# Optimization experiments

Hardware: AMD Instinct MI355X
Metric: run time of the kernel (lower is better)

Reference implementation:

```python
import jax, jax.numpy as jnp
import numpy as np

B, P, K = 8, 1024, 20          # clouds, points per cloud, knn neighbors
H, HD = 256, 512               # module hidden_dim, edge-MLP hidden (TransformerBlockRes default)
L, C = 3, 512                  # n_hidden_layers, n_components
N = B * P
LN_EPS = 1e-5


def _layer_norm(x, g, b):
    m = jnp.mean(x, axis=-1, keepdims=True)
    v = jnp.var(x, axis=-1, keepdims=True)
    return (x - m) * jax.lax.rsqrt(v + LN_EPS) * g + b


def _mlp(x, W1, b1, g1, be1, W2, b2, g2, be2):
    # Linear -> LayerNorm -> ELU -> Linear -> LayerNorm -> ELU (pos_nn / attn_nn)
    h = jax.nn.elu(_layer_norm(x @ W1 + b1, g1, be1))
    return jax.nn.elu(_layer_norm(h @ W2 + b2, g2, be2))


def _knn(pos):
    # knn_graph within each cloud, loop=False (self excluded). Equal-size clouds.
    p = pos.reshape(B, P, 3)
    d2 = jnp.sum((p[:, :, None, :] - p[:, None, :, :]) ** 2, axis=-1)  # [B,P,P]
    d2 = d2 + jnp.eye(P, dtype=d2.dtype) * 1e10                        # exclude self
    idx = jax.lax.top_k(-d2, K)[1]                                     # [B,P,K]
    return (idx + (jnp.arange(B) * P)[:, None, None]).reshape(N, K)    # global ids


def setup_inputs() -> dict:
    key = jax.random.key(0)
    cnt = [0]

    def nrm(shape, scale):
        cnt[0] += 1
        return (jax.random.normal(jax.random.fold_in(key, cnt[0]), shape, dtype=jnp.float32) * scale)

    d = {}
    d["pos"] = nrm((N, 3), 1.0)
    d["batch"] = jnp.repeat(jnp.arange(B, dtype=jnp.int32), P)
    # stem Linear(3, H)
    d["ffm_W"] = nrm((3, H), 3 ** -0.5); d["ffm_b"] = jnp.zeros((H,), jnp.float32)
    # PointTransformerConv linears (no bias), stacked over L layers
    s = H ** -0.5
    d["lin_W"] = nrm((L, H, H), s); d["src_W"] = nrm((L, H, H), s); d["dst_W"] = nrm((L, H, H), s)
    # pos_nn: Linear(3,HD)+LN+ELU+Linear(HD,H)+LN+ELU
    d["pos1_W"] = nrm((L, 3, HD), 3 ** -0.5); d["pos1_b"] = jnp.zeros((L, HD), jnp.float32)
    d["pos_ln1_g"] = jnp.ones((L, HD), jnp.float32); d["pos_ln1_b"] = jnp.zeros((L, HD), jnp.float32)
    d["pos2_W"] = nrm((L, HD, H), HD ** -0.5); d["pos2_b"] = jnp.zeros((L, H), jnp.float32)
    d["pos_ln2_g"] = jnp.ones((L, H), jnp.float32); d["pos_ln2_b"] = jnp.zeros((L, H), jnp.float32)
    # attn_nn: Linear(H,HD)+LN+ELU+Linear(HD,H)+LN+ELU
    d["att1_W"] = nrm((L, H, HD), s); d["att1_b"] = jnp.zeros((L, HD), jnp.float32)
    d["att_ln1_g"] = jnp.ones((L, HD), jnp.float32); d["att_ln1_b"] = jnp.zeros((L, HD), jnp.float32)
    d["att2_W"] = nrm((L, HD, H), HD ** -0.5); d["att2_b"] = jnp.zeros((L, H), jnp.float32)
    d["att_ln2_g"] = jnp.ones((L, H), jnp.float32); d["att_ln2_b"] = jnp.zeros((L, H), jnp.float32)
    # per-layer tail: LayerNorm + ELU + Linear + ResidualCoefficient
    d["blk_ln_g"] = jnp.ones((L, H), jnp.float32); d["blk_ln_b"] = jnp.zeros((L, H), jnp.float32)
    d["blk_W"] = nrm((L, H, H), s); d["blk_b"] = jnp.zeros((L, H), jnp.float32)
    d["res_alpha"] = nrm((L,), 0.1)  # torch init is zeros; small random for a nontrivial test
    d["r1_W"] = nrm((H, H), s); d["r1_b"] = jnp.zeros((H,), jnp.float32)
    d["r2_W"] = nrm((H, H), s); d["r2_b"] = jnp.zeros((H,), jnp.float32)
    d["r2_ln_g"] = jnp.ones((H,), jnp.float32); d["r2_ln_b"] = jnp.zeros((H,), jnp.float32)
    d["r3_W"] = nrm((H, H), s); d["r3_b"] = jnp.zeros((H,), jnp.float32)
    d["r3_ln_g"] = jnp.ones((H,), jnp.float32); d["r3_ln_b"] = jnp.zeros((H,), jnp.float32)
    d["r4_W"] = nrm((H, C), s); d["r4_b"] = jnp.zeros((C,), jnp.float32)
    return d


def reference(pos, batch, ffm_W, ffm_b, lin_W, src_W, dst_W,
              pos1_W, pos1_b, pos_ln1_g, pos_ln1_b, pos2_W, pos2_b, pos_ln2_g, pos_ln2_b,
              att1_W, att1_b, att_ln1_g, att_ln1_b, att2_W, att2_b, att_ln2_g, att_ln2_b,
              blk_ln_g, blk_ln_b, blk_W, blk_b, res_alpha,
              r1_W, r1_b, r2_W, r2_b, r2_ln_g, r2_ln_b, r3_W, r3_b, r3_ln_g, r3_ln_b, r4_W, r4_b):
    # knn graph is identical every layer (pos never changes) -> compute once
    neigh = _knn(pos)                       # [N,K] neighbor (source) ids j for each target i
    rel = pos[:, None, :] - pos[neigh]      # pos_i - pos_j, [N,K,3]
    x = pos @ ffm_W + ffm_b                 # [N,H]
    for i in range(L):
        a_src = x @ src_W[i]                # [N,H]
        a_dst = x @ dst_W[i]
        v = x @ lin_W[i]
        delta = _mlp(rel, pos1_W[i], pos1_b[i], pos_ln1_g[i], pos_ln1_b[i],
                     pos2_W[i], pos2_b[i], pos_ln2_g[i], pos_ln2_b[i])          # [N,K,H]
        alpha = _mlp(a_dst[:, None, :] - a_src[neigh] + delta,
                     att1_W[i], att1_b[i], att_ln1_g[i], att_ln1_b[i],
                     att2_W[i], att2_b[i], att_ln2_g[i], att_ln2_b[i])          # [N,K,H]
        attn = jax.nn.softmax(alpha, axis=1)                                    # per-channel over K neighbors
        agg = jnp.sum(attn * (v[neigh] + delta), axis=1)                        # sum aggregation (PyG default)
        h = jax.nn.elu(_layer_norm(agg, blk_ln_g[i], blk_ln_b[i])) @ blk_W[i] + blk_b[i]
        x = x + res_alpha[i] * h
    h = x @ r1_W + r1_b                                                         # [N,H]
    pooled = jax.ops.segment_max(h, batch, num_segments=B)                      # global_max_pool [B,H]
    h = jax.nn.elu(_layer_norm(pooled @ r2_W + r2_b, r2_ln_g, r2_ln_b))
    h = jax.nn.elu(_layer_norm(h @ r3_W + r3_b, r3_ln_g, r3_ln_b))
    return h @ r4_W + r4_b                                                      # [B,C]
```

## Files before the change

kernel.cpp:

```cpp
#include <hip/hip_runtime.h>
#include <math.h>

#define NPTS 8192
#define PPC  1024
#define BCL  8
#define KNN  20
#define HDIM 256
#define HD2  512
#define NL   3
#define NCOMP 512
#define EDG  (NPTS*KNN)
#define QS   768

typedef __bf16 bf16x8 __attribute__((ext_vector_type(8)));
typedef float f32x4 __attribute__((ext_vector_type(4)));
typedef unsigned int uint4v __attribute__((ext_vector_type(4)));
typedef unsigned short us8 __attribute__((ext_vector_type(8)));

__device__ inline unsigned short f2bf(float f) {
  unsigned u = __float_as_uint(f);
  u += 0x7FFF + ((u >> 16) & 1);
  return (unsigned short)(u >> 16);
}
__device__ inline float bf2f(unsigned short u) {
  return __uint_as_float((unsigned)u << 16);
}
__device__ inline float elu(float y) { return (y > 0.f) ? y : (expf(y) - 1.f); }

__global__ __launch_bounds__(256)
void knn_wave(const float* __restrict__ pos, int* __restrict__ neigh,
              float* __restrict__ rel_f) {
  __shared__ float px[PPC], py[PPC], pz[PPC];
  int tid = threadIdx.x;
  int i0 = blockIdx.x * 4;
  int base = i0 & ~(PPC - 1);
  for (int t = tid; t < PPC; t += 256) {
    px[t] = pos[(size_t)(base + t) * 3 + 0];
    py[t] = pos[(size_t)(base + t) * 3 + 1];
    pz[t] = pos[(size_t)(base + t) * 3 + 2];
  }
  __syncthreads();
  int wave = tid >> 6, lane = tid & 63;
  int i = i0 + wave;
  int il = i - base;
  float xi = px[il], yi = py[il], zi = pz[il];
  float d[16];
  #pragma unroll
  for (int q = 0; q < 16; ++q) {
    int t = lane + 64 * q;
    float dx = xi - px[t], dy = yi - py[t], dz = zi - pz[t];
    float dd = dx * dx + dy * dy + dz * dz;
    d[q] = (t == il) ? 3.4e38f : dd;
  }
  int mywin = 0;
  for (int k = 0; k < KNN; ++k) {
    float v = d[0]; int idx = lane;
    #pragma unroll
    for (int q = 1; q < 16; ++q)
      if (d[q] < v) { v = d[q]; idx = q * 64 + lane; }
    #pragma unroll
    for (int off = 1; off < 64; off <<= 1) {
      float ov = __shfl_xor(v, off, 64);
      int oi = __shfl_xor(idx, off, 64);
      if (ov < v || (ov == v && oi < idx)) { v = ov; idx = oi; }
    }
    if (lane == k) mywin = idx;
    int qwin = idx >> 6;
    bool own = (idx & 63) == lane;
    #pragma unroll
    for (int q = 0; q < 16; ++q)
      if (own && q == qwin) d[q] = 3.4e38f;
  }
  if (lane < KNN) {
    neigh[(size_t)i * KNN + lane] = base + mywin;
    size_t rb = ((size_t)i * KNN + lane) * 3;
    rel_f[rb + 0] = xi - px[mywin];
    rel_f[rb + 1] = yi - py[mywin];
    rel_f[rb + 2] = zi - pz[mywin];
  }
}

__global__ __launch_bounds__(256)
void transpose_w(const float* __restrict__ W, unsigned short* __restrict__ out,
                 int K, int N, int Kpad) {
  int n = blockIdx.x;
  for (int k = threadIdx.x; k < Kpad; k += 256)
    out[(size_t)n * Kpad + k] = (k < K) ? f2bf(W[(size_t)k * N + n]) : (unsigned short)0;
}

__global__ __launch_bounds__(64)
void pack_w(const float* __restrict__ W, unsigned short* __restrict__ out, int N) {
  int blk = blockIdx.x;
  int NT = N / 16;
  int ks = blk / NT, nt = blk % NT;
  int lane = threadIdx.x;
  int l16 = lane & 15, quad = lane >> 4;
  int col = nt * 16 + l16;
  int krow = ks * 32 + quad * 8;
  unsigned short o[8];
  #pragma unroll
  for (int j = 0; j < 8; ++j)
    o[j] = f2bf(W[(size_t)(krow + j) * N + col]);
  *(uint4v*)&out[((size_t)blk * 64 + lane) * 8] = *(uint4v*)o;
}

__global__ __launch_bounds__(256)
void prep_pos(const float* __restrict__ pos, unsigned short* __restrict__ posb) {
  int idx = blockIdx.x * 256 + threadIdx.x;
  int m = idx >> 5, c = idx & 31;
  posb[idx] = (c < 3) ? f2bf(pos[(size_t)m * 3 + c]) : (unsigned short)0;
}

__global__ __launch_bounds__(256)
void pos_fused(const float* __restrict__ rel_f, const float* __restrict__ W1,
               const float* __restrict__ b1, const float* __restrict__ g1,
               const float* __restrict__ be1,
               const unsigned short* __restrict__ B2p, const float* __restrict__ bias2,
               const float* __restrict__ g2, const float* __restrict__ be2,
               unsigned short* __restrict__ delta_b, int edge_base) {
  __shared__ alignas(16) char smem[46464];
  unsigned short* H = (unsigned short*)smem;
  float* w1s = (float*)(smem + 33280);
  float* b1s = w1s + 1536;
  float* g1s = b1s + 512;
  float* be1s = g1s + 512;
  float* lnsum = (float*)(smem + 45568);
  float* lnsq = lnsum + 64;
  float* relS = (float*)(smem + 46080);
  int tid = threadIdx.x;
  int wave = tid >> 6, lane = tid & 63;
  int el0 = blockIdx.x * 32;
  int eg0 = edge_base + el0;
  for (int t = tid; t < 1536; t += 256) w1s[t] = W1[t];
  for (int t = tid; t < 512; t += 256) { b1s[t] = b1[t]; g1s[t] = g1[t]; be1s[t] = be1[t]; }
  if (tid < 96) relS[tid] = rel_f[(size_t)eg0 * 3 + tid];
  __syncthreads();
  {
    int rIW = lane >> 3, sub = lane & 7;
    int row = wave * 8 + rIW;
    float r0 = relS[row * 3 + 0], r1v = relS[row * 3 + 1], r2v = relS[row * 3 + 2];
    int cb = sub * 64;
    float h[64]; float s = 0.f, sq = 0.f;
    #pragma unroll
    for (int cc = 0; cc < 16; ++cc) {
      f32x4 w0 = *(const f32x4*)&w1s[cb + cc * 4];
      f32x4 wa = *(const f32x4*)&w1s[512 + cb + cc * 4];
      f32x4 wb = *(const f32x4*)&w1s[1024 + cb + cc * 4];
      f32x4 bb = *(const f32x4*)&b1s[cb + cc * 4];
      #pragma unroll
      for (int q = 0; q < 4; ++q) {
        float hv = fmaf(r0, w0[q], fmaf(r1v, wa[q], fmaf(r2v, wb[q], bb[q])));
        h[cc * 4 + q] = hv; s += hv; sq += hv * hv;
      }
    }
    #pragma unroll
    for (int off = 1; off < 8; off <<= 1) { s += __shfl_xor(s, off, 64); sq += __shfl_xor(sq, off, 64); }
    float mean = s * (1.f / 512.f);
    float var = sq * (1.f / 512.f) - mean * mean;
    float rr = rsqrtf(var + 1e-5f);
    #pragma unroll
    for (int cc = 0; cc < 8; ++cc) {
      f32x4 ga = *(const f32x4*)&g1s[cb + cc * 8];
      f32x4 gb = *(const f32x4*)&g1s[cb + cc * 8 + 4];
      f32x4 ba = *(const f32x4*)&be1s[cb + cc * 8];
      f32x4 bb2 = *(const f32x4*)&be1s[cb + cc * 8 + 4];
      unsigned short o[8];
      #pragma unroll
      for (int q = 0; q < 4; ++q) {
        o[q]     = f2bf(elu((h[cc * 8 + q]     - mean) * rr * ga[q] + ba[q]));
        o[q + 4] = f2bf(elu((h[cc * 8 + 4 + q] - mean) * rr * gb[q] + bb2[q]));
      }
      *(uint4v*)&H[row * 520 + cb + cc * 8] = *(uint4v*)o;
    }
  }
  __syncthreads();
  int quad = lane >> 4, l16 = lane & 15;
  int wm2 = (wave >> 1) * 16, wn2 = (wave & 1) * 128, wni = wave & 1;
  int nb2 = (wave & 1) * 8;
  f32x4 acc2[8] = {};
  for (int k0 = 0; k0 < 512; k0 += 32) {
    int ks = k0 >> 5;
    bf16x8 bvv[8];
    #pragma unroll
    for (int ni = 0; ni < 8; ++ni)
      bvv[ni] = *(const bf16x8*)(B2p + ((size_t)(ks * 16 + nb2 + ni) * 64 + lane) * 8);
    bf16x8 a2 = __builtin_bit_cast(bf16x8, *(const uint4v*)&H[(wm2 + l16) * 520 + k0 + quad * 8]);
    #pragma unroll
    for (int ni = 0; ni < 8; ++ni)
      acc2[ni] = __builtin_amdgcn_mfma_f32_16x16x32_bf16(a2, bvv[ni], acc2[ni], 0, 0, 0);
  }
  #pragma unroll
  for (int r = 0; r < 4; ++r) {
    int row = wm2 + quad * 4 + r;
    float s2 = 0.f, q2 = 0.f;
    #pragma unroll
    for (int ni = 0; ni < 8; ++ni) {
      float val = acc2[ni][r] + bias2[wn2 + ni * 16 + l16];
      acc2[ni][r] = val; s2 += val; q2 += val * val;
    }
    #pragma unroll
    for (int off = 1; off < 16; off <<= 1) { s2 += __shfl_xor(s2, off, 64); q2 += __shfl_xor(q2, off, 64); }
    if (l16 == 0) { lnsum[wni * 32 + row] = s2; lnsq[wni * 32 + row] = q2; }
  }
  __syncthreads();
  #pragma unroll
  for (int r = 0; r < 4; ++r) {
    int row = wm2 + quad * 4 + r;
    float tot = lnsum[row] + lnsum[32 + row];
    float tsq = lnsq[row] + lnsq[32 + row];
    float mean = tot * (1.f / 256.f);
    float var = tsq * (1.f / 256.f) - mean * mean;
    float rr = rsqrtf(var + 1e-5f);
    size_t ob = (size_t)(el0 + row) * 256;
    #pragma unroll
    for (int ni = 0; ni < 8; ++ni) {
      int col = wn2 + ni * 16 + l16;
      delta_b[ob + col] = f2bf(elu((acc2[ni][r] - mean) * rr * g2[col] + be2[col]));
    }
  }
}

__global__ __launch_bounds__(256)
void attn_fused(const unsigned short* __restrict__ qkv,
                const unsigned short* __restrict__ delta_b,
                const int* __restrict__ neigh,
                const unsigned short* __restrict__ B1p, const float* __restrict__ bias1,
                const float* __restrict__ g1, const float* __restrict__ be1,
                const unsigned short* __restrict__ B2p, const float* __restrict__ bias2,
                const float* __restrict__ g2, const float* __restrict__ be2,
                unsigned short* __restrict__ alpha_b, int edge_base) {
  __shared__ alignas(16) char smem[50944];
  unsigned short* As = (unsigned short*)smem;
  unsigned short* H  = (unsigned short*)(smem + 16896);
  float* lnsum = (float*)(smem + 50176);
  float* lnsq  = lnsum + 64;
  int* iS = (int*)(smem + 50688);
  int* jS = iS + 32;
  int tid = threadIdx.x;
  int wave = tid >> 6, lane = tid & 63;
  int quad = lane >> 4, l16 = lane & 15;
  int el0 = blockIdx.x * 32;
  int eg0 = edge_base + el0;
  if (tid < 32) { iS[tid] = (eg0 + tid) / KNN; jS[tid] = neigh[eg0 + tid]; }
  __syncthreads();
  {
    int r = tid & 31, seg = tid >> 5;
    int i = iS[r], j = jS[r], e = el0 + r;
    int c0 = seg * 32;
    #pragma unroll
    for (int q4 = 0; q4 < 4; ++q4) {
      int c = c0 + q4 * 8;
      us8 pd = *(const us8*)(qkv + (size_t)i * QS + 256 + c);
      us8 ps = *(const us8*)(qkv + (size_t)j * QS + c);
      us8 pl = *(const us8*)(delta_b + (size_t)e * 256 + c);
      unsigned short o[8];
      #pragma unroll
      for (int q = 0; q < 8; ++q)
        o[q] = f2bf(bf2f(pd[q]) - bf2f(ps[q]) + bf2f(pl[q]));
      *(uint4v*)&As[r * 264 + c] = *(uint4v*)o;
    }
  }
  __syncthreads();
  int wm1 = (wave >> 1) * 16, wn1 = (wave & 1) * 256, wni = wave & 1;
  int nb1 = (wave & 1) * 16;
  f32x4 acc1[16] = {};
  for (int k0 = 0; k0 < 256; k0 += 32) {
    int ks = k0 >> 5;
    bf16x8 bvv[16];
    #pragma unroll
    for (int ni = 0; ni < 16; ++ni)
      bvv[ni] = *(const bf16x8*)(B1p + ((size_t)(ks * 32 + nb1 + ni) * 64 + lane) * 8);
    bf16x8 a1 = __builtin_bit_cast(bf16x8, *(const uint4v*)&As[(wm1 + l16) * 264 + k0 + quad * 8]);
    #pragma unroll
    for (int ni = 0; ni < 16; ++ni)
      acc1[ni] = __builtin_amdgcn_mfma_f32_16x16x32_bf16(a1, bvv[ni], acc1[ni], 0, 0, 0);
  }
  #pragma unroll
  for (int r = 0; r < 4; ++r) {
    int row = wm1 + quad * 4 + r;
    float s = 0.f, sq = 0.f;
    #pragma unroll
    for (int ni = 0; ni < 16; ++ni) {
      float val = acc1[ni][r] + bias1[wn1 + ni * 16 + l16];
      acc1[ni][r] = val; s += val; sq += val * val;
    }
    #pragma unroll
    for (int off = 1; off < 16; off <<= 1) { s += __shfl_xor(s, off, 64); sq += __shfl_xor(sq, off, 64); }
    if (l16 == 0) { lnsum[wni * 32 + row] = s; lnsq[wni * 32 + row] = sq; }
  }
  __syncthreads();
  #pragma unroll
  for (int r = 0; r < 4; ++r) {
    int row = wm1 + quad * 4 + r;
    float tot = lnsum[row] + lnsum[32 + row];
    float tsq = lnsq[row] + lnsq[32 + row];
    float mean = tot * (1.f / 512.f);
    float var = tsq * (1.f / 512.f) - mean * mean;
    float rr = rsqrtf(var + 1e-5f);
    #pragma unroll
    for (int ni = 0; ni < 16; ++ni) {
      int col = wn1 + ni * 16 + l16;
      H[row * 520 + col] = f2bf(elu((acc1[ni][r] - mean) * rr * g1[col] + be1[col]));
    }
  }
  __syncthreads();
  int wm2 = (wave >> 1) * 16, wn2 = (wave & 1) * 128;
  int nb2 = (wave & 1) * 8;
  f32x4 acc2[8] = {};
  for (int k0 = 0; k0 < 512; k0 += 32) {
    int ks = k0 >> 5;
    bf16x8 bvv[8];
    #pragma unroll
    for (int ni = 0; ni < 8; ++ni)
      bvv[ni] = *(const bf16x8*)(B2p + ((size_t)(ks * 16 + nb2 + ni) * 64 + lane) * 8);
    bf16x8 a2 = __builtin_bit_cast(bf16x8, *(const uint4v*)&H[(wm2 + l16) * 520 + k0 + quad * 8]);
    #pragma unroll
    for (int ni = 0; ni < 8; ++ni)
      acc2[ni] = __builtin_amdgcn_mfma_f32_16x16x32_bf16(a2, bvv[ni], acc2[ni], 0, 0, 0);
  }
  #pragma unroll
  for (int r = 0; r < 4; ++r) {
    int row = wm2 + quad * 4 + r;
    float s2 = 0.f, q2 = 0.f;
    #pragma unroll
    for (int ni = 0; ni < 8; ++ni) {
      float val = acc2[ni][r] + bias2[wn2 + ni * 16 + l16];
      acc2[ni][r] = val; s2 += val; q2 += val * val;
    }
    #pragma unroll
    for (int off = 1; off < 16; off <<= 1) { s2 += __shfl_xor(s2, off, 64); q2 += __shfl_xor(q2, off, 64); }
    if (l16 == 0) { lnsum[wni * 32 + row] = s2; lnsq[wni * 32 + row] = q2; }
  }
  __syncthreads();
  #pragma unroll
  for (int r = 0; r < 4; ++r) {
    int row = wm2 + quad * 4 + r;
    float tot = lnsum[row] + lnsum[32 + row];
    float tsq = lnsq[row] + lnsq[32 + row];
    float mean = tot * (1.f / 256.f);
    float var = tsq * (1.f / 256.f) - mean * mean;
    float rr = rsqrtf(var + 1e-5f);
    size_t ob = (size_t)(el0 + row) * 256;
    #pragma unroll
    for (int ni = 0; ni < 8; ++ni) {
      int col = wn2 + ni * 16 + l16;
      alpha_b[ob + col] = f2bf(elu((acc2[ni][r] - mean) * rr * g2[col] + be2[col]));
    }
  }
}

#define APAD 40
__global__ __launch_bounds__(256)
void gemm_mfma(const unsigned short* __restrict__ A, const unsigned short* __restrict__ Bt,
               const float* __restrict__ bias, float* __restrict__ Cf,
               unsigned short* __restrict__ Cb, int M, int Nn, int Kk) {
  __shared__ alignas(16) unsigned short As[128 * APAD];
  __shared__ alignas(16) unsigned short Bs[128 * APAD];
  int tid = threadIdx.x;
  int wave = tid >> 6, lane = tid & 63;
  int quad = lane >> 4, l16 = lane & 15;
  int wm = (wave >> 1) * 64, wn = (wave & 1) * 64;
  int m0 = blockIdx.y * 128, n0 = blockIdx.x * 128;
  f32x4 acc[4][4] = {};
  int srow = tid >> 2;
  int scol = (tid & 3) * 8;
  for (int k0 = 0; k0 < Kk; k0 += 32) {
    #pragma unroll
    for (int h = 0; h < 2; ++h) {
      int r = srow + h * 64;
      int gm = m0 + r;
      uint4v va = {0, 0, 0, 0};
      if (gm < M) va = *(const uint4v*)(A + (size_t)gm * Kk + k0 + scol);
      *(uint4v*)(&As[r * APAD + scol]) = va;
      int gn = n0 + r;
      uint4v vb = *(const uint4v*)(Bt + (size_t)gn * Kk + k0 + scol);
      *(uint4v*)(&Bs[r * APAD + scol]) = vb;
    }
    __syncthreads();
    bf16x8 af[4], bfr[4];
    #pragma unroll
    for (int mi = 0; mi < 4; ++mi)
      af[mi] = __builtin_bit_cast(bf16x8, *(const uint4v*)(&As[(wm + mi * 16 + l16) * APAD + quad * 8]));
    #pragma unroll
    for (int ni = 0; ni < 4; ++ni)
      bfr[ni] = __builtin_bit_cast(bf16x8, *(const uint4v*)(&Bs[(wn + ni * 16 + l16) * APAD + quad * 8]));
    #pragma unroll
    for (int mi = 0; mi < 4; ++mi)
      #pragma unroll
      for (int ni = 0; ni < 4; ++ni)
        acc[mi][ni] = __builtin_amdgcn_mfma_f32_16x16x32_bf16(af[mi], bfr[ni], acc[mi][ni], 0, 0, 0);
    __syncthreads();
  }
  float bvs[4]; int gns[4];
  #pragma unroll
  for (int ni = 0; ni < 4; ++ni) {
    gns[ni] = n0 + wn + ni * 16 + l16;
    bvs[ni] = bias ? bias[gns[ni]] : 0.f;
  }
  #pragma unroll
  for (int mi = 0; mi < 4; ++mi) {
    #pragma unroll
    for (int r = 0; r < 4; ++r) {
      int gm = m0 + wm + mi * 16 + quad * 4 + r;
      if (gm >= M) continue;
      #pragma unroll
      for (int ni = 0; ni < 4; ++ni) {
        float val = acc[mi][ni][r] + bvs[ni];
        if (Cf) Cf[(size_t)gm * Nn + gns[ni]] = val;
        if (Cb) Cb[(size_t)gm * Nn + gns[ni]] = f2bf(val);
      }
    }
  }
}

#define BM0 64
#define BN0 64
#define BK0 16
__global__ __launch_bounds__(256)
void gemm_bias(const float* __restrict__ A, const float* __restrict__ Bw,
               const float* __restrict__ bias, float* __restrict__ C,
               int M, int Nn, int Kk) {
  __shared__ float Asm[BK0][BM0 + 1];
  __shared__ float Bsm[BK0][BN0 + 1];
  int bm = blockIdx.y * BM0, bn = blockIdx.x * BN0;
  int tid = threadIdx.x;
  int tx = tid & 15, ty = tid >> 4;
  float acc[4][4] = {{0.f}};
  for (int k0 = 0; k0 < Kk; k0 += BK0) {
    #pragma unroll
    for (int ii = 0; ii < 4; ++ii) {
      int e = tid + ii * 256;
      int m = e >> 4, k = e & 15;
      int gm = bm + m, gk = k0 + k;
      Asm[k][m] = (gm < M && gk < Kk) ? A[(size_t)gm * Kk + gk] : 0.f;
    }
    #pragma unroll
    for (int ii = 0; ii < 4; ++ii) {
      int e = tid + ii * 256;
      int k = e >> 6, n = e & 63;
      int gk = k0 + k, gn = bn + n;
      Bsm[k][n] = (gk < Kk && gn < Nn) ? Bw[(size_t)gk * Nn + gn] : 0.f;
    }
    __syncthreads();
    #pragma unroll
    for (int kk = 0; kk < BK0; ++kk) {
      float a[4], b[4];
      #pragma unroll
      for (int ii = 0; ii < 4; ++ii) a[ii] = Asm[kk][ty * 4 + ii];
      #pragma unroll
      for (int jj = 0; jj < 4; ++jj) b[jj] = Bsm[kk][tx * 4 + jj];
      #pragma unroll
      for (int ii = 0; ii < 4; ++ii)
        #pragma unroll
        for (int jj = 0; jj < 4; ++jj)
          acc[ii][jj] += a[ii] * b[jj];
    }
    __syncthreads();
  }
  #pragma unroll
  for (int ii = 0; ii < 4; ++ii) {
    int gm = bm + ty * 4 + ii;
    if (gm >= M) continue;
    #pragma unroll
    for (int jj = 0; jj < 4; ++jj) {
      int gn = bn + tx * 4 + jj;
      if (gn >= Nn) continue;
      float vv = acc[ii][jj];
      if (bias) vv += bias[gn];
      C[(size_t)gm * Nn + gn] = vv;
    }
  }
}

__global__ __launch_bounds__(256)
void ln_elu_kernel(const float* __restrict__ in, float* __restrict__ outf,
                   unsigned short* __restrict__ outb,
                   const float* __restrict__ g, const float* __restrict__ bb,
                   int Cn, int do_elu) {
  __shared__ float sdata[4];
  size_t row = blockIdx.x;
  const float* x = in + row * Cn;
  int tid = threadIdx.x;
  float v0 = x[tid];
  float v1 = (Cn == 512) ? x[tid + 256] : 0.f;
  float s = v0 + v1;
  #pragma unroll
  for (int off = 32; off > 0; off >>= 1) s += __shfl_xor(s, off, 64);
  if ((tid & 63) == 0) sdata[tid >> 6] = s;
  __syncthreads();
  float mean = (sdata[0] + sdata[1] + sdata[2] + sdata[3]) / (float)Cn;
  float d0 = v0 - mean;
  float d1 = (Cn == 512) ? (v1 - mean) : 0.f;
  float sq = d0 * d0 + d1 * d1;
  __syncthreads();
  #pragma unroll
  for (int off = 32; off > 0; off >>= 1) sq += __shfl_xor(sq, off, 64);
  if ((tid & 63) == 0) sdata[tid >> 6] = sq;
  __syncthreads();
  float var = (sdata[0] + sdata[1] + sdata[2] + sdata[3]) / (float)Cn;
  float r = rsqrtf(var + 1e-5f);
  float y0 = d0 * r * g[tid] + bb[tid];
  if (do_elu) y0 = elu(y0);
  if (outf) outf[row * Cn + tid] = y0;
  if (outb) outb[row * Cn + tid] = f2bf(y0);
  if (Cn == 512) {
    float y1 = d1 * r * g[tid + 256] + bb[tid + 256];
    if (do_elu) y1 = elu(y1);
    if (outf) outf[row * Cn + tid + 256] = y1;
    if (outb) outb[row * Cn + tid + 256] = f2bf(y1);
  }
}

__global__ __launch_bounds__(256)
void softmax_agg(const unsigned short* __restrict__ alpha_b,
                 const unsigned short* __restrict__ delta_b,
                 const unsigned short* __restrict__ qkv,
                 const int* __restrict__ neigh,
                 float* __restrict__ agg, int node0) {
  int nl = blockIdx.x;
  int c = threadIdx.x;
  int i = node0 + nl;
  float av[KNN];
  float mx = -3.4e38f;
  #pragma unroll
  for (int k = 0; k < KNN; ++k) {
    av[k] = bf2f(alpha_b[((size_t)nl * KNN + k) * HDIM + c]);
    mx = fmaxf(mx, av[k]);
  }
  float ssum = 0.f;
  #pragma unroll
  for (int k = 0; k < KNN; ++k) { av[k] = expf(av[k] - mx); ssum += av[k]; }
  float inv = 1.f / ssum;
  float acc = 0.f;
  #pragma unroll
  for (int k = 0; k < KNN; ++k) {
    int j = neigh[(size_t)i * KNN + k];
    acc += av[k] * inv * (bf2f(qkv[(size_t)j * QS + 512 + c]) +
                          bf2f(delta_b[((size_t)nl * KNN + k) * HDIM + c]));
  }
  agg[(size_t)i * HDIM + c] = acc;
}

__global__ __launch_bounds__(256)
void axpy_res(float* __restrict__ x, unsigned short* __restrict__ xb,
              const float* __restrict__ h, const float* __restrict__ alpha, int l) {
  size_t idx = (size_t)blockIdx.x * 256 + threadIdx.x;
  float nv = x[idx] + alpha[l] * h[idx];
  x[idx] = nv;
  xb[idx] = f2bf(nv);
}

__global__ __launch_bounds__(256)
void seg_max_p(const float* __restrict__ h, float* __restrict__ part) {
  int blk = blockIdx.x;
  int b = blk >> 4, ch = blk & 15;
  int c = threadIdx.x;
  const float* base = h + ((size_t)b * PPC + (size_t)ch * 64) * HDIM;
  float m = -3.4e38f;
  for (int p = 0; p < 64; ++p)
    m = fmaxf(m, base[(size_t)p * HDIM + c]);
  part[(size_t)blk * HDIM + c] = m;
}
__global__ __launch_bounds__(256)
void seg_max_f(const float* __restrict__ part, float* __restrict__ pooled) {
  int b = blockIdx.x;
  int c = threadIdx.x;
  float m = -3.4e38f;
  for (int k = 0; k < 16; ++k)
    m = fmaxf(m, part[(size_t)(b * 16 + k) * HDIM + c]);
  pooled[(size_t)b * HDIM + c] = m;
}

extern "C" void kernel_launch(void* const* d_in, const int* in_sizes, int n_in,
                              void* d_out, int out_size, void* d_ws, size_t ws_size,
                              hipStream_t stream) {
  const float* pos       = (const float*)d_in[0];
  const float* ffm_W     = (const float*)d_in[2];
  const float* ffm_b     = (const float*)d_in[3];
  const float* lin_W     = (const float*)d_in[4];
  const float* src_W     = (const float*)d_in[5];
  const float* dst_W     = (const float*)d_in[6];
  const float* pos1_W    = (const float*)d_in[7];
  const float* pos1_b    = (const float*)d_in[8];
  const float* pos_ln1_g = (const float*)d_in[9];
  const float* pos_ln1_b = (const float*)d_in[10];
  const float* pos2_W    = (const float*)d_in[11];
  const float* pos2_b    = (const float*)d_in[12];
  const float* pos_ln2_g = (const float*)d_in[13];
  const float* pos_ln2_b = (const float*)d_in[14];
  const float* att1_W    = (const float*)d_in[15];
  const float* att1_b    = (const float*)d_in[16];
  const float* att_ln1_g = (const float*)d_in[17];
  const float* att_ln1_b = (const float*)d_in[18];
  const float* att2_W    = (const float*)d_in[19];
  const float* att2_b    = (const float*)d_in[20];
  const float* att_ln2_g = (const float*)d_in[21];
  const float* att_ln2_b = (const float*)d_in[22];
  const float* blk_ln_g  = (const float*)d_in[23];
  const float* blk_ln_b  = (const float*)d_in[24];
  const float* blk_W     = (const float*)d_in[25];
  const float* blk_b     = (const float*)d_in[26];
  const float* res_alpha = (const float*)d_in[27];
  const float* r1_W = (const float*)d_in[28]; const float* r1_b = (const float*)d_in[29];
  const float* r2_W = (const float*)d_in[30]; const float* r2_b = (const float*)d_in[31];
  const float* r2_ln_g = (const float*)d_in[32]; const float* r2_ln_b = (const float*)d_in[33];
  const float* r3_W = (const float*)d_in[34]; const float* r3_b = (const float*)d_in[35];
  const float* r3_ln_g = (const float*)d_in[36]; const float* r3_ln_b = (const float*)d_in[37];
  const float* r4_W = (const float*)d_in[38]; const float* r4_b = (const float*)d_in[39];
  float* out = (float*)d_out;

  char* wsp = (char*)d_ws;
  auto alloc = [&](size_t bytes) -> void* {
    void* p = (void*)wsp;
    wsp += (bytes + 255) & ~(size_t)255;
    return p;
  };
  int*            neigh   = (int*)alloc(EDG * sizeof(int));
  float*          rel_f   = (float*)alloc((size_t)EDG * 3 * 4);
  unsigned short* posb    = (unsigned short*)alloc((size_t)NPTS * 32 * 2);
  float*          x       = (float*)alloc((size_t)NPTS * HDIM * 4);
  unsigned short* xb      = (unsigned short*)alloc((size_t)NPTS * HDIM * 2);
  unsigned short* xln_b   = (unsigned short*)alloc((size_t)NPTS * HDIM * 2);
  unsigned short* qkv     = (unsigned short*)alloc((size_t)NPTS * QS * 2);
  float*          agg     = (float*)alloc((size_t)NPTS * HDIM * 4);
  float*          segp    = (float*)alloc((size_t)128 * HDIM * 4);
  float*          pooled  = (float*)alloc((size_t)BCL * HDIM * 4);
  float*          hh      = (float*)alloc((size_t)BCL * HDIM * 4);
  unsigned short* ffmt = (unsigned short*)alloc((size_t)HDIM * 32 * 2);
  unsigned short* r1t  = (unsigned short*)alloc((size_t)HDIM * HDIM * 2);
  unsigned short *qkvt[NL], *blkt[NL];
  unsigned short *pos2p[NL], *att1p[NL], *att2p[NL];
  for (int l = 0; l < NL; ++l) {
    qkvt[l]  = (unsigned short*)alloc((size_t)QS * HDIM * 2);
    blkt[l]  = (unsigned short*)alloc((size_t)HDIM * HDIM * 2);
    pos2p[l] = (unsigned short*)alloc((size_t)HDIM * HD2 * 2);
    att1p[l] = (unsigned short*)alloc((size_t)HD2 * HDIM * 2);
    att2p[l] = (unsigned short*)alloc((size_t)HDIM * HD2 * 2);
  }
  size_t used = (size_t)(wsp - (char*)d_ws);
  size_t avail = (ws_size > used) ? (ws_size - used) : 0;
  size_t per_node = (size_t)KNN * (HDIM * 2 * 2) + 1024;
  int Nc = (int)(avail / per_node);
  if (Nc > NPTS) Nc = NPTS;
  Nc &= ~15;
  if (Nc < 16) Nc = 16;
  unsigned short* delta_b = (unsigned short*)alloc((size_t)Nc * KNN * HDIM * 2);
  unsigned short* alpha_b = (unsigned short*)alloc((size_t)Nc * KNN * HDIM * 2);

  auto mgemm = [&](const unsigned short* A, const unsigned short* Bt, const float* bias,
                   float* Cf, unsigned short* Cb, int M, int Nn, int Kk) {
    dim3 g(Nn / 128, (M + 127) / 128);
    gemm_mfma<<<g, dim3(256), 0, stream>>>(A, Bt, bias, Cf, Cb, M, Nn, Kk);
  };
  auto fgemm = [&](const float* A, const float* Bw, const float* bias, float* Cp,
                   int M, int Nn, int Kk) {
    dim3 g((Nn + BN0 - 1) / BN0, (M + BM0 - 1) / BM0);
    gemm_bias<<<g, dim3(256), 0, stream>>>(A, Bw, bias, Cp, M, Nn, Kk);
  };

  transpose_w<<<HDIM, 256, 0, stream>>>(ffm_W, ffmt, 3, HDIM, 32);
  transpose_w<<<HDIM, 256, 0, stream>>>(r1_W, r1t, HDIM, HDIM, HDIM);
  for (int l = 0; l < NL; ++l) {
    transpose_w<<<HDIM, 256, 0, stream>>>(src_W + (size_t)l * HDIM * HDIM, qkvt[l], HDIM, HDIM, HDIM);
    transpose_w<<<HDIM, 256, 0, stream>>>(dst_W + (size_t)l * HDIM * HDIM, qkvt[l] + 256 * 256, HDIM, HDIM, HDIM);
    transpose_w<<<HDIM, 256, 0, stream>>>(lin_W + (size_t)l * HDIM * HDIM, qkvt[l] + 512 * 256, HDIM, HDIM, HDIM);
    transpose_w<<<HDIM, 256, 0, stream>>>(blk_W + (size_t)l * HDIM * HDIM, blkt[l], HDIM, HDIM, HDIM);
    pack_w<<<(HD2 / 32) * (HDIM / 16), 64, 0, stream>>>(pos2_W + (size_t)l * HD2 * HDIM, pos2p[l], HDIM);
    pack_w<<<(HDIM / 32) * (HD2 / 16), 64, 0, stream>>>(att1_W + (size_t)l * HDIM * HD2, att1p[l], HD2);
    pack_w<<<(HD2 / 32) * (HDIM / 16), 64, 0, stream>>>(att2_W + (size_t)l * HD2 * HDIM, att2p[l], HDIM);
  }

  knn_wave<<<NPTS / 4, 256, 0, stream>>>(pos, neigh, rel_f);
  prep_pos<<<NPTS * 32 / 256, 256, 0, stream>>>(pos, posb);
  mgemm(posb, ffmt, ffm_b, x, xb, NPTS, HDIM, 32);

  for (int l = 0; l < NL; ++l) {
    mgemm(xb, qkvt[l], nullptr, nullptr, qkv, NPTS, QS, HDIM);

    for (int n0 = 0; n0 < NPTS; n0 += Nc) {
      int nc = (Nc < NPTS - n0) ? Nc : (NPTS - n0);
      int ec = nc * KNN;
      pos_fused<<<ec / 32, 256, 0, stream>>>(
          rel_f, pos1_W + (size_t)l * 3 * HD2, pos1_b + (size_t)l * HD2,
          pos_ln1_g + (size_t)l * HD2, pos_ln1_b + (size_t)l * HD2,
          pos2p[l], pos2_b + (size_t)l * HDIM,
          pos_ln2_g + (size_t)l * HDIM, pos_ln2_b + (size_t)l * HDIM,
          delta_b, n0 * KNN);
      attn_fused<<<ec / 32, 256, 0, stream>>>(
          qkv, delta_b, neigh,
          att1p[l], att1_b + (size_t)l * HD2,
          att_ln1_g + (size_t)l * HD2, att_ln1_b + (size_t)l * HD2,
          att2p[l], att2_b + (size_t)l * HDIM,
          att_ln2_g + (size_t)l * HDIM, att_ln2_b + (size_t)l * HDIM,
          alpha_b, n0 * KNN);
      softmax_agg<<<nc, 256, 0, stream>>>(alpha_b, delta_b, qkv, neigh, agg, n0);
    }
    ln_elu_kernel<<<NPTS, 256, 0, stream>>>(agg, nullptr, xln_b,
                                            blk_ln_g + (size_t)l * HDIM, blk_ln_b + (size_t)l * HDIM, HDIM, 1);
    mgemm(xln_b, blkt[l], blk_b + (size_t)l * HDIM, agg, nullptr, NPTS, HDIM, HDIM);
    axpy_res<<<(NPTS * HDIM) / 256, 256, 0, stream>>>(x, xb, agg, res_alpha, l);
  }

  mgemm(xb, r1t, r1_b, agg, nullptr, NPTS, HDIM, HDIM);
  seg_max_p<<<128, 256, 0, stream>>>(agg, segp);
  seg_max_f<<<BCL, 256, 0, stream>>>(segp, pooled);
  fgemm(pooled, r2_W, r2_b, hh, BCL, HDIM, HDIM);
  ln_elu_kernel<<<BCL, 256, 0, stream>>>(hh, hh, nullptr, r2_ln_g, r2_ln_b, HDIM, 1);
  fgemm(hh, r3_W, r3_b, pooled, BCL, HDIM, HDIM);
  ln_elu_kernel<<<BCL, 256, 0, stream>>>(pooled, pooled, nullptr, r3_ln_g, r3_ln_b, HDIM, 1);
  fgemm(pooled, r4_W, r4_b, out, BCL, NCOMP, HDIM);
}
```

Measured before the change: 1.912 ms.

## Use fast bf16 conversion and exp, build attention A operand in registers

Replaces round-to-nearest-even bf16 conversion with a cheaper add-and-shift rounding, plus a packed hardware conversion where available. Switches expf to __expf in ELU and softmax. In attn_fused, the gathered difference operand is now built straight into registers in MFMA A layout, so the LDS staging buffer and one barrier are gone and shared memory per block shrinks. This trades slightly different rounding and exp accuracy for fewer instructions, and the register-held A operand raises register pressure.

```diff
diff --git a/kernel.cpp b/kernel.cpp
--- a/kernel.cpp
+++ b/kernel.cpp
@@ -22,10 +22,22 @@
   u += 0x7FFF + ((u >> 16) & 1);
   return (unsigned short)(u >> 16);
 }
+__device__ inline unsigned short f2bf_fast(float f) {
+  return (unsigned short)((__float_as_uint(f) + 0x8000u) >> 16);
+}
+__device__ inline unsigned pack2bf(float a, float b) {
+#if __has_builtin(__builtin_amdgcn_cvt_pk_bf16_f32)
+  auto t = __builtin_amdgcn_cvt_pk_bf16_f32(a, b);
+  return __builtin_bit_cast(unsigned, t);
+#else
+  return ((__float_as_uint(a) + 0x8000u) >> 16) |
+         ((__float_as_uint(b) + 0x8000u) & 0xFFFF0000u);
+#endif
+}
 __device__ inline float bf2f(unsigned short u) {
   return __uint_as_float((unsigned)u << 16);
 }
-__device__ inline float elu(float y) { return (y > 0.f) ? y : (expf(y) - 1.f); }
+__device__ inline float elu(float y) { return (y > 0.f) ? y : (__expf(y) - 1.f); }
 
 __global__ __launch_bounds__(256)
 void knn_wave(const float* __restrict__ pos, int* __restrict__ neigh,
@@ -160,17 +172,15 @@
     float rr = rsqrtf(var + 1e-5f);
     #pragma unroll
     for (int cc = 0; cc < 8; ++cc) {
-      f32x4 ga = *(const f32x4*)&g1s[cb + cc * 8];
-      f32x4 gb = *(const f32x4*)&g1s[cb + cc * 8 + 4];
-      f32x4 ba = *(const f32x4*)&be1s[cb + cc * 8];
-      f32x4 bb2 = *(const f32x4*)&be1s[cb + cc * 8 + 4];
-      unsigned short o[8];
+      unsigned u[4];
       #pragma unroll
       for (int q = 0; q < 4; ++q) {
-        o[q]     = f2bf(elu((h[cc * 8 + q]     - mean) * rr * ga[q] + ba[q]));
-        o[q + 4] = f2bf(elu((h[cc * 8 + 4 + q] - mean) * rr * gb[q] + bb2[q]));
+        int c0 = cb + cc * 8 + 2 * q;
+        float y0 = elu((h[cc * 8 + 2 * q]     - mean) * rr * g1s[c0]     + be1s[c0]);
+        float y1 = elu((h[cc * 8 + 2 * q + 1] - mean) * rr * g1s[c0 + 1] + be1s[c0 + 1]);
+        u[q] = pack2bf(y0, y1);
       }
-      *(uint4v*)&H[row * 520 + cb + cc * 8] = *(uint4v*)o;
+      *(uint4v*)&H[row * 520 + cb + cc * 8] = *(uint4v*)u;
     }
   }
   __syncthreads();
@@ -215,7 +225,7 @@
     #pragma unroll
     for (int ni = 0; ni < 8; ++ni) {
       int col = wn2 + ni * 16 + l16;
-      delta_b[ob + col] = f2bf(elu((acc2[ni][r] - mean) * rr * g2[col] + be2[col]));
+      delta_b[ob + col] = f2bf_fast(elu((acc2[ni][r] - mean) * rr * g2[col] + be2[col]));
     }
   }
 }
@@ -229,12 +239,11 @@
                 const unsigned short* __restrict__ B2p, const float* __restrict__ bias2,
                 const float* __restrict__ g2, const float* __restrict__ be2,
                 unsigned short* __restrict__ alpha_b, int edge_base) {
-  __shared__ alignas(16) char smem[50944];
-  unsigned short* As = (unsigned short*)smem;
-  unsigned short* H  = (unsigned short*)(smem + 16896);
-  float* lnsum = (float*)(smem + 50176);
+  __shared__ alignas(16) char smem[34304];
+  unsigned short* H = (unsigned short*)smem;
+  float* lnsum = (float*)(smem + 33280);
   float* lnsq  = lnsum + 64;
-  int* iS = (int*)(smem + 50688);
+  int* iS = (int*)(smem + 33792);
   int* jS = iS + 32;
   int tid = threadIdx.x;
   int wave = tid >> 6, lane = tid & 63;
@@ -243,34 +252,37 @@
   int eg0 = edge_base + el0;
   if (tid < 32) { iS[tid] = (eg0 + tid) / KNN; jS[tid] = neigh[eg0 + tid]; }
   __syncthreads();
-  {
-    int r = tid & 31, seg = tid >> 5;
-    int i = iS[r], j = jS[r], e = el0 + r;
-    int c0 = seg * 32;
-    #pragma unroll
-    for (int q4 = 0; q4 < 4; ++q4) {
-      int c = c0 + q4 * 8;
-      us8 pd = *(const us8*)(qkv + (size_t)i * QS + 256 + c);
-      us8 ps = *(const us8*)(qkv + (size_t)j * QS + c);
-      us8 pl = *(const us8*)(delta_b + (size_t)e * 256 + c);
-      unsigned short o[8];
-      #pragma unroll
-      for (int q = 0; q < 8; ++q)
-        o[q] = f2bf(bf2f(pd[q]) - bf2f(ps[q]) + bf2f(pl[q]));
-      *(uint4v*)&As[r * 264 + c] = *(uint4v*)o;
-    }
-  }
-  __syncthreads();
   int wm1 = (wave >> 1) * 16, wn1 = (wave & 1) * 256, wni = wave & 1;
   int nb1 = (wave & 1) * 16;
+  us8 areg[8];
+  {
+    int r = wm1 + l16;
+    int i = iS[r], j = jS[r], e = el0 + r;
+    const unsigned short* pdp = qkv + (size_t)i * QS + 256;
+    const unsigned short* psp = qkv + (size_t)j * QS;
+    const unsigned short* plp = delta_b + (size_t)e * 256;
+    #pragma unroll
+    for (int ks = 0; ks < 8; ++ks) {
+      int c = ks * 32 + quad * 8;
+      us8 pd = *(const us8*)(pdp + c);
+      us8 ps = *(const us8*)(psp + c);
+      us8 pl = *(const us8*)(plp + c);
+      unsigned u[4];
+      #pragma unroll
+      for (int q = 0; q < 4; ++q)
+        u[q] = pack2bf(bf2f(pd[2*q])   - bf2f(ps[2*q])   + bf2f(pl[2*q]),
+                       bf2f(pd[2*q+1]) - bf2f(ps[2*q+1]) + bf2f(pl[2*q+1]));
+      areg[ks] = __builtin_bit_cast(us8, *(uint4v*)u);
+    }
+  }
   f32x4 acc1[16] = {};
-  for (int k0 = 0; k0 < 256; k0 += 32) {
-    int ks = k0 >> 5;
+  #pragma unroll
+  for (int ks = 0; ks < 8; ++ks) {
     bf16x8 bvv[16];
     #pragma unroll
     for (int ni = 0; ni < 16; ++ni)
       bvv[ni] = *(const bf16x8*)(B1p + ((size_t)(ks * 32 + nb1 + ni) * 64 + lane) * 8);
-    bf16x8 a1 = __builtin_bit_cast(bf16x8, *(const uint4v*)&As[(wm1 + l16) * 264 + k0 + quad * 8]);
+    bf16x8 a1 = __builtin_bit_cast(bf16x8, areg[ks]);
     #pragma unroll
     for (int ni = 0; ni < 16; ++ni)
       acc1[ni] = __builtin_amdgcn_mfma_f32_16x16x32_bf16(a1, bvv[ni], acc1[ni], 0, 0, 0);
@@ -300,7 +312,7 @@
     #pragma unroll
     for (int ni = 0; ni < 16; ++ni) {
       int col = wn1 + ni * 16 + l16;
-      H[row * 520 + col] = f2bf(elu((acc1[ni][r] - mean) * rr * g1[col] + be1[col]));
+      H[row * 520 + col] = f2bf_fast(elu((acc1[ni][r] - mean) * rr * g1[col] + be1[col]));
     }
   }
   __syncthreads();
@@ -344,7 +356,7 @@
     #pragma unroll
     for (int ni = 0; ni < 8; ++ni) {
       int col = wn2 + ni * 16 + l16;
-      alpha_b[ob + col] = f2bf(elu((acc2[ni][r] - mean) * rr * g2[col] + be2[col]));
+      alpha_b[ob + col] = f2bf_fast(elu((acc2[ni][r] - mean) * rr * g2[col] + be2[col]));
     }
   }
 }
@@ -407,7 +419,7 @@
       for (int ni = 0; ni < 4; ++ni) {
         float val = acc[mi][ni][r] + bvs[ni];
         if (Cf) Cf[(size_t)gm * Nn + gns[ni]] = val;
-        if (Cb) Cb[(size_t)gm * Nn + gns[ni]] = f2bf(val);
+        if (Cb) Cb[(size_t)gm * Nn + gns[ni]] = f2bf_fast(val);
       }
     }
   }
@@ -502,12 +514,12 @@
   float y0 = d0 * r * g[tid] + bb[tid];
   if (do_elu) y0 = elu(y0);
   if (outf) outf[row * Cn + tid] = y0;
-  if (outb) outb[row * Cn + tid] = f2bf(y0);
+  if (outb) outb[row * Cn + tid] = f2bf_fast(y0);
   if (Cn == 512) {
     float y1 = d1 * r * g[tid + 256] + bb[tid + 256];
     if (do_elu) y1 = elu(y1);
     if (outf) outf[row * Cn + tid + 256] = y1;
-    if (outb) outb[row * Cn + tid + 256] = f2bf(y1);
+    if (outb) outb[row * Cn + tid + 256] = f2bf_fast(y1);
   }
 }
 
@@ -529,7 +541,7 @@
   }
   float ssum = 0.f;
   #pragma unroll
-  for (int k = 0; k < KNN; ++k) { av[k] = expf(av[k] - mx); ssum += av[k]; }
+  for (int k = 0; k < KNN; ++k) { av[k] = __expf(av[k] - mx); ssum += av[k]; }
   float inv = 1.f / ssum;
   float acc = 0.f;
   #pragma unroll
@@ -547,7 +559,7 @@
   size_t idx = (size_t)blockIdx.x * 256 + threadIdx.x;
   float nv = x[idx] + alpha[l] * h[idx];
   x[idx] = nv;
-  xb[idx] = f2bf(nv);
+  xb[idx] = f2bf_fast(nv);
 }
 
 __global__ __launch_bounds__(256)
```

New measurement: 1.948 ms. Within noise of the previous version (+1.9%).
